# Performance work log

Hardware: AMD Instinct MI355X
Metric: run time of the kernel (lower is better)

The kernel has to match this reference:

```python
import jax, jax.numpy as jnp
import numpy as np

BN_EPS = 1e-5
LN_EPS = 1e-5


def conv1d(x, w, b):
    # x: (B, Cin, L), w: (Cout, Cin, K) 'same' padding
    pad = (w.shape[-1] - 1) // 2
    y = jax.lax.conv_general_dilated(x, w, (1,), [(pad, pad)],
                                     dimension_numbers=('NCH', 'OIH', 'NCH'))
    return y + b[None, :, None]


def bn_eval(x, g, b):
    # BatchNorm1d in eval mode with running_mean=0, running_var=1
    scale = g / np.float32(np.sqrt(1.0 + BN_EPS))
    return x * scale[None, :, None] + b[None, :, None]


def dss_kernel(lam_re, lam_im, log_dt, W_re, W_im, L):
    # lam_*: (N,), log_dt: (H,), W_*: (2, H, N) -> K: (2, H, L) real
    Lam = -jnp.exp(lam_re) + 1j * lam_im                  # (N,) stable poles
    dt = jnp.exp(log_dt)                                   # (H,)
    dtL = dt[:, None] * Lam[None, :]                       # (H, N)
    # ZOH-style input discretization folded into W
    Wc = (W_re + 1j * W_im) * ((jnp.exp(dtL) - 1.0) / Lam[None, :])[None]  # (2,H,N)
    pos = jnp.arange(L, dtype=jnp.float32)
    E = jnp.exp(dtL[:, :, None] * pos[None, None, :])      # (H, N, L) complex Vandermonde
    return jnp.einsum('chn,hnl->chl', Wc, E).real          # (2, H, L)


def dss_layer(x, lam_re, lam_im, log_dt, W_re, W_im, D, out_w, out_b):
    # x: (B, H, L) transposed DSS block, bidirectional, postact='glu'
    B, H, L = x.shape
    K = dss_kernel(lam_re, lam_im, log_dt, W_re, W_im, L)  # (2, H, L)
    zpad = jnp.zeros_like(K[0])
    k = (jnp.concatenate([K[0], zpad], -1) +
         jnp.concatenate([zpad, K[1][..., ::-1]], -1))     # (H, 2L) bidirectional kernel
    k_f = jnp.fft.rfft(k, axis=-1)                          # (H, L+1)
    u_f = jnp.fft.rfft(x, n=2 * L, axis=-1)                 # (B, H, L+1)
    y = jnp.fft.irfft(k_f[None] * u_f, n=2 * L, axis=-1)[..., :L]
    y = y + D[None, :, None] * x                            # skip term
    y = jax.nn.gelu(y, approximate=False)
    y = jnp.einsum('oh,bhl->bol', out_w, y) + out_b[None, :, None]  # (B, 2H, L)
    a, g = jnp.split(y, 2, axis=1)
    return a * jax.nn.sigmoid(g)                            # GLU -> (B, H, L)


def layernorm_ch(x, g, b):
    # LayerNorm over channel dim of (B, H, L)
    mu = x.mean(axis=1, keepdims=True)
    var = ((x - mu) ** 2).mean(axis=1, keepdims=True)
    return (x - mu) / jnp.sqrt(var + LN_EPS) * g[None, :, None] + b[None, :, None]


def reference(x, enc_w, enc_b, rn_w1, rn_b1, rn_g1, rn_be1, rn_w2, rn_b2, rn_g2,
              rn_be2, lam_re, lam_im, log_dt, W_re, W_im, D, out_w, out_b,
              ln_g, ln_b, dec_w, dec_b):
    x = conv1d(x, enc_w, enc_b)                             # (B, H, L)
    for i in range(rn_w1.shape[0]):                         # resnet L1Blocks
        z = jax.nn.relu(bn_eval(conv1d(x, rn_w1[i], rn_b1[i]), rn_g1[i], rn_be1[i]))
        z = bn_eval(conv1d(z, rn_w2[i], rn_b2[i]), rn_g2[i], rn_be2[i])
        x = jax.nn.relu(z + x)
    for i in range(lam_re.shape[0]):                        # DSS blocks (post-norm)
        z = dss_layer(x, lam_re[i], lam_im[i], log_dt[i], W_re[i], W_im[i],
                      D[i], out_w[i], out_b[i])
        x = layernorm_ch(z + x, ln_g[i], ln_b[i])
    return conv1d(x, dec_w, dec_b)                          # (B, d_output, L)


def setup_inputs() -> dict:
    key = jax.random.key(0)
    ks = jax.random.split(key, 12)
    B, L, H, N = 16, 8192, 128, 32
    nl, nr = 4, 3
    f = lambda k, shape, s=1.0: jax.random.normal(k, shape, dtype=jnp.float32) * np.float32(s)
    x = f(ks[0], (B, 5, L))
    enc_w = f(ks[1], (H, 5, 15), 1.0 / np.sqrt(5 * 15)); enc_b = jnp.zeros((H,), jnp.float32)
    rn_w1 = f(ks[2], (nr, H, H, 7), 1.0 / np.sqrt(H * 7)); rn_b1 = jnp.zeros((nr, H), jnp.float32)
    rn_w2 = f(ks[3], (nr, H, H, 7), 1.0 / np.sqrt(H * 7)); rn_b2 = jnp.zeros((nr, H), jnp.float32)
    rn_g1 = jnp.ones((nr, H), jnp.float32); rn_be1 = jnp.zeros((nr, H), jnp.float32)
    rn_g2 = jnp.ones((nr, H), jnp.float32); rn_be2 = jnp.zeros((nr, H), jnp.float32)
    lam_re = f(ks[4], (nl, N), 0.5)
    lam_im = jnp.pi * jnp.arange(N, dtype=jnp.float32)[None, :] * jnp.ones((nl, 1), jnp.float32)
    log_dt = f(ks[5], (nl, H), 0.5) - 4.0
    W_re = f(ks[6], (nl, 2, H, N), 1.0 / np.sqrt(N))
    W_im = f(ks[7], (nl, 2, H, N), 1.0 / np.sqrt(N))
    D = f(ks[8], (nl, H))
    out_w = f(ks[9], (nl, 2 * H, H), 1.0 / np.sqrt(H)); out_b = jnp.zeros((nl, 2 * H), jnp.float32)
    ln_g = jnp.ones((nl, H), jnp.float32); ln_b = jnp.zeros((nl, H), jnp.float32)
    dec_w = f(ks[10], (5, H, 15), 1.0 / np.sqrt(H * 15)); dec_b = jnp.zeros((5,), jnp.float32)
    return {'x': x, 'enc_w': enc_w, 'enc_b': enc_b, 'rn_w1': rn_w1, 'rn_b1': rn_b1,
            'rn_g1': rn_g1, 'rn_be1': rn_be1, 'rn_w2': rn_w2, 'rn_b2': rn_b2,
            'rn_g2': rn_g2, 'rn_be2': rn_be2, 'lam_re': lam_re, 'lam_im': lam_im,
            'log_dt': log_dt, 'W_re': W_re, 'W_im': W_im, 'D': D, 'out_w': out_w,
            'out_b': out_b, 'ln_g': ln_g, 'ln_b': ln_b, 'dec_w': dec_w, 'dec_b': dec_b}
```

## Files before the change

### kernel.cpp

```cpp
#include <hip/hip_runtime.h>
#include <hip/hip_bf16.h>


#define BN   16
#define HCH  128
#define LSEQ 8192
#define NST  32
#define NLAY 4
#define XT_BSTRIDE 2101248ull

typedef __attribute__((ext_vector_type(4))) float f32x4;
typedef __attribute__((ext_vector_type(8))) short short8;
typedef unsigned short u16;
typedef unsigned int   u32;

struct __align__(8) U2 { u32 x, y; };
struct __align__(16) US8 { u16 v[8]; };
struct __align__(8) US4 { u16 v[4]; };

__device__ __forceinline__ u16 f2bf(float f){
  union { float f; u32 u; } v; v.f = f;
  u32 u = v.u;
  return (u16)((u + 0x7fffu + ((u >> 16) & 1u)) >> 16);
}
__device__ __forceinline__ float bf2f(u32 lo16){
  union { u32 u; float f; } v; v.u = lo16 << 16; return v.f;
}
__device__ __forceinline__ float geluf(float v){
  return 0.5f * v * (1.0f + erff(v * 0.70710678118654752f));
}

#define GLDS16(g, l) \
  __builtin_amdgcn_global_load_lds((const __attribute__((address_space(1))) u32*)(g), \
                                   (__attribute__((address_space(3))) u32*)(l), 16, 0, 0)

__global__ void k_xpad(u16* xTs){
  int b = blockIdx.x, t = threadIdx.x;
  char* base = (char*)xTs + (size_t)b * XT_BSTRIDE;
  int r = t >> 4;
  int row = (r < 8) ? r : (8192 + r);
  f32x4 z = {0.f, 0.f, 0.f, 0.f};
  *(f32x4*)(base + (size_t)row * 256 + (size_t)(t & 15) * 16) = z;
}

__global__ void k_wxform(const float* __restrict__ w1, const float* __restrict__ w2, u16* __restrict__ wswz){
  int idx = blockIdx.x * 256 + threadIdx.x;
  if (idx >= 6 * 128 * 896) return;
  int conv = idx / (128 * 896);
  int rem  = idx % (128 * 896);
  int co = rem / 896, K = rem % 896;
  int k = K >> 7, ci = K & 127;
  const float* src = (conv & 1) ? w2 : w1;
  int blk = conv >> 1;
  float v = src[(((size_t)blk * 128 + co) * 128 + ci) * 7 + k];
  int chunk = K >> 6, j = K & 63;
  size_t byteoff = (size_t)conv * 229376 + (size_t)chunk * 16384 + (size_t)co * 128
                 + (u32)((j * 2) ^ ((co & 7) << 4));
  *(u16*)((char*)wswz + byteoff) = f2bf(v);
}

__global__ void k_wdec(const float* __restrict__ dw, u16* __restrict__ wd){
  int idx = blockIdx.x * 256 + threadIdx.x;
  if (idx >= 16 * 1920) return;
  int co = idx / 1920, K = idx % 1920;
  int k = K >> 7, ci = K & 127;
  float v = (co < 5) ? dw[((size_t)co * 128 + ci) * 15 + k] : 0.f;
  size_t byteoff = (size_t)co * 3840 + (u32)((K * 2) ^ ((co & 7) << 4));
  *(u16*)((char*)wd + byteoff) = f2bf(v);
}

__global__ void k_wglu(const float* __restrict__ ow, u16* __restrict__ wg){
  int idx = blockIdx.x * 256 + threadIdx.x;
  if (idx >= NLAY * 256 * 128) return;
  int layer = idx >> 15;
  int rem = idx & 32767;
  int q = rem >> 7, k = rem & 127;
  int row = (q & 1) ? (128 + (q >> 1)) : (q >> 1);
  float v = ow[((size_t)layer * 256 + row) * 128 + k];
  u16 hb = f2bf(v);
  u16 lb = f2bf(v - bf2f(hb));
  int a_hi = k >> 6, kk = k & 63;
  size_t base = (size_t)layer * 131072 + (size_t)q * 128 + (u32)((kk * 2) ^ ((q & 7) << 4));
  *(u16*)((char*)wg + base + (size_t)a_hi * 32768) = hb;
  *(u16*)((char*)wg + base + (size_t)(2 + a_hi) * 32768) = lb;
}

__global__ void k_dssprep(const float* __restrict__ lam_re, const float* __restrict__ lam_im,
                          const float* __restrict__ log_dt, const float* __restrict__ W_re,
                          const float* __restrict__ W_im, float* __restrict__ dssp){
  int idx = blockIdx.x * 256 + threadIdx.x;
  if (idx >= NLAY * HCH * NST) return;
  int layer = idx / (HCH * NST);
  int hn = idx % (HCH * NST);
  int h = hn / NST, n = hn % NST;
  float Lre = -expf(lam_re[layer * NST + n]);
  float Lim = lam_im[layer * NST + n];
  float dt  = expf(log_dt[layer * HCH + h]);
  float are = dt * Lre, aim = dt * Lim;
  float er = expf(are);
  float rre = er * cosf(aim);
  float rim = er * sinf(aim);
  float nre = rre - 1.f, nim = rim;
  float den = 1.f / (Lre * Lre + Lim * Lim);
  float fre = (nre * Lre + nim * Lim) * den;
  float fim = (nim * Lre - nre * Lim) * den;
  float* base = dssp + (size_t)layer * 6 * HCH * NST;
  base[(0 * HCH + h) * NST + n] = rre;
  base[(1 * HCH + h) * NST + n] = rim;
  #pragma unroll
  for (int cc = 0; cc < 2; ++cc){
    float wr_ = W_re[(((size_t)layer * 2 + cc) * HCH + h) * NST + n];
    float wi_ = W_im[(((size_t)layer * 2 + cc) * HCH + h) * NST + n];
    base[((2 + 2 * cc) * HCH + h) * NST + n] = wr_ * fre - wi_ * fim;
    base[((3 + 2 * cc) * HCH + h) * NST + n] = wr_ * fim + wi_ * fre;
  }
}

__global__ __launch_bounds__(256) void k_mats(const float* __restrict__ pp,
                                              u16* __restrict__ A1c, u16* __restrict__ A2c,
                                              float* __restrict__ rC){
  int h = blockIdx.x, t = threadIdx.x;
  __shared__ float pre[129][33], pim[129][33];
  __shared__ float w0re[32], w0im[32], w1re[32], w1im[32];
  __shared__ float tf[128], tb[128];
  if (t < 32){
    int n = t;
    float rre = pp[(0 * HCH + h) * NST + n], rim = pp[(1 * HCH + h) * NST + n];
    w0re[n] = pp[(2 * HCH + h) * NST + n]; w0im[n] = pp[(3 * HCH + h) * NST + n];
    w1re[n] = pp[(4 * HCH + h) * NST + n]; w1im[n] = pp[(5 * HCH + h) * NST + n];
    float pr = 1.f, pi = 0.f;
    pre[0][n] = 1.f; pim[0][n] = 0.f;
    for (int p = 1; p <= 128; ++p){
      float nr = pr * rre - pi * rim;
      float ni = pr * rim + pi * rre;
      pr = nr; pi = ni;
      pre[p][n] = pr; pim[p][n] = pi;
    }
    rC[h * 64 + 2 * n] = pr; rC[h * 64 + 2 * n + 1] = pi;
  }
  __syncthreads();
  if (t < 128){
    float s = 0.f;
    for (int n = 0; n < 32; ++n) s += w0re[n] * pre[t][n] - w0im[n] * pim[t][n];
    tf[t] = s;
  } else {
    int d = t - 128;
    if (d == 0) tb[0] = 0.f;
    else {
      float s = 0.f;
      for (int n = 0; n < 32; ++n) s += w1re[n] * pre[d - 1][n] - w1im[n] * pim[d - 1][n];
      tb[d] = s;
    }
  }
  __syncthreads();
  for (int idx = t; idx < 4 * 128 * 64; idx += 256){
    int a = idx >> 13, rem = idx & 8191, q = rem >> 6, k = rem & 63;
    int j = (a & 1) * 64 + k;
    int n, p; float wr_, wi_;
    if (q < 64){ n = q >> 1; p = 127 - j; wr_ = w0re[n]; wi_ = w0im[n]; }
    else       { n = (q - 64) >> 1; p = j; wr_ = w1re[n]; wi_ = w1im[n]; }
    float pr = pre[p][n], pi = pim[p][n];
    float v = (q & 1) ? (wr_ * pi + wi_ * pr) : (wr_ * pr - wi_ * pi);
    u16 hb = f2bf(v);
    u16 ob = (a < 2) ? hb : f2bf(v - bf2f(hb));
    *(u16*)((char*)A1c + (size_t)h * 65536 + (size_t)a * 16384 + (size_t)q * 128
            + (u32)((k * 2) ^ ((q & 7) << 4))) = ob;
  }
  for (int idx = t; idx < 8 * 128 * 64; idx += 256){
    int a = idx >> 13, rem = idx & 8191, i = rem >> 6, k = rem & 63;
    float v; bool lo;
    if (a < 4){
      int colT = (a & 1) * 64 + k;
      v = (i >= colT) ? tf[i - colT] : tb[colT - i];
      lo = (a >= 2);
    } else {
      int n = k >> 1;
      int p = (a < 6) ? (i + 1) : (127 - i);
      v = (k & 1) ? -pim[p][n] : pre[p][n];
      lo = (a == 5) || (a == 7);
    }
    u16 hb = f2bf(v);
    u16 ob = lo ? f2bf(v - bf2f(hb)) : hb;
    *(u16*)((char*)A2c + (size_t)h * 131072 + (size_t)a * 16384 + (size_t)i * 128
            + (u32)((k * 2) ^ ((i & 7) << 4))) = ob;
  }
}

__global__ __launch_bounds__(128) void k_enc(const float* __restrict__ xin, const float* __restrict__ w,
                                             const float* __restrict__ bias, float* __restrict__ X){
  int b = blockIdx.y, l0 = blockIdx.x * 64;
  int t = threadIdx.x;
  __shared__ float xs[5][78];
  for (int i = t; i < 5 * 78; i += 128){
    int ci = i / 78, j = i % 78;
    int l = l0 - 7 + j;
    xs[ci][j] = (l >= 0 && l < LSEQ) ? xin[((size_t)b * 5 + ci) * LSEQ + l] : 0.f;
  }
  float wreg[75];
  #pragma unroll
  for (int i = 0; i < 75; ++i) wreg[i] = w[t * 75 + i];
  float bc = bias[t];
  __syncthreads();
  size_t orow = ((size_t)b * HCH + t) * LSEQ + l0;
  for (int gb = 0; gb < 8; ++gb){
    float acc[8] = {0, 0, 0, 0, 0, 0, 0, 0};
    #pragma unroll
    for (int ci = 0; ci < 5; ++ci){
      #pragma unroll
      for (int k = 0; k < 15; ++k){
        float wv = wreg[ci * 15 + k];
        #pragma unroll
        for (int j = 0; j < 8; ++j)
          acc[j] = fmaf(wv, xs[ci][gb * 8 + j + k], acc[j]);
      }
    }
    f32x4 o0 = {acc[0] + bc, acc[1] + bc, acc[2] + bc, acc[3] + bc};
    f32x4 o1 = {acc[4] + bc, acc[5] + bc, acc[6] + bc, acc[7] + bc};
    *(f32x4*)&X[orow + gb * 8]     = o0;
    *(f32x4*)&X[orow + gb * 8 + 4] = o1;
  }
}

__global__ __launch_bounds__(256) void k_xform(const float* __restrict__ Xin, u16* __restrict__ xTs){
  int b = blockIdx.y, l0 = blockIdx.x * 64;
  int t = threadIdx.x;
  __shared__ float tile[128][65];
  #pragma unroll
  for (int it = 0; it < 32; ++it){
    int idx = t + it * 256;
    int ci = idx >> 6, j = idx & 63;
    tile[ci][j] = Xin[((size_t)b * HCH + ci) * LSEQ + l0 + j];
  }
  __syncthreads();
  int rl = t >> 2, q = t & 3;
  int l = l0 + rl;
  char* rowp = (char*)xTs + (size_t)b * XT_BSTRIDE + (size_t)(l + 8) * 256;
  u32 key = ((u32)l & 7u) << 4;
  #pragma unroll
  for (int ii = 0; ii < 8; ++ii){
    int c0 = q * 32 + ii * 4;
    U2 val;
    val.x = (u32)f2bf(tile[c0 + 0][rl]) | ((u32)f2bf(tile[c0 + 1][rl]) << 16);
    val.y = (u32)f2bf(tile[c0 + 2][rl]) | ((u32)f2bf(tile[c0 + 3][rl]) << 16);
    *(U2*)(rowp + (((u32)(c0 * 2)) ^ key)) = val;
  }
}

__global__ __launch_bounds__(256, 2) void k_conv(
    const u16* __restrict__ xTs, const u16* __restrict__ wcv,
    const float* __restrict__ bng, const float* __restrict__ bnb, const float* __restrict__ bnbe,
    const float* __restrict__ Xres, float* __restrict__ Xout, u16* __restrict__ xTsOut)
{
  int b = blockIdx.y, l0 = blockIdx.x * 128;
  int tid = threadIdx.x, lane = tid & 63, wv = tid >> 6;
  int wr = wv >> 1, wc = wv & 1;
  int lan15 = lane & 15, lhi = lane >> 4;

  __shared__ alignas(16) u16 xt[144 * 128];
  __shared__ alignas(16) u16 wch[2][128 * 64];

  const char* xsrc = (const char*)xTs + (size_t)b * XT_BSTRIDE + (size_t)l0 * 256;
  #pragma unroll
  for (int is = 0; is < 9; ++is){
    int off = is * 4096 + wv * 1024;
    GLDS16(xsrc + off + (lane << 4), (char*)xt + off);
  }
  {
    const char* wsrc = (const char*)wcv;
    #pragma unroll
    for (int is = 0; is < 4; ++is){
      int off = is * 4096 + wv * 1024;
      GLDS16(wsrc + off + (lane << 4), (char*)&wch[0][0] + off);
    }
  }
  asm volatile("s_waitcnt vmcnt(0)" ::: "memory");
  __syncthreads();

  f32x4 acc[4][4];
  #pragma unroll
  for (int i = 0; i < 4; ++i)
    #pragma unroll
    for (int j = 0; j < 4; ++j) acc[i][j] = (f32x4){0.f, 0.f, 0.f, 0.f};

  for (int c = 0; c < 14; ++c){
    int cur = c & 1;
    if (c < 13){
      const char* wsrc = (const char*)wcv + (size_t)(c + 1) * 16384;
      #pragma unroll
      for (int is = 0; is < 4; ++is){
        int off = is * 4096 + wv * 1024;
        GLDS16(wsrc + off + (lane << 4), (char*)&wch[cur ^ 1][0] + off);
      }
    }
    int k = c >> 1;
    const char* wb = (const char*)&wch[cur][0];
    #pragma unroll
    for (int ks = 0; ks < 2; ++ks){
      short8 af[4], bf[4];
      int j0 = ks * 32 + lhi * 8;
      #pragma unroll
      for (int mt = 0; mt < 4; ++mt){
        int co = wr * 64 + mt * 16 + lan15;
        af[mt] = *(const short8*)(wb + co * 128 + ((j0 * 2) ^ ((co & 7) << 4)));
      }
      int ci0 = (c & 1) * 64 + ks * 32 + lhi * 8;
      #pragma unroll
      for (int nt = 0; nt < 4; ++nt){
        int ll = wc * 64 + nt * 16 + lan15;
        int row = ll + k + 5;
        int lg = l0 + ll + k - 3;
        bf[nt] = *(const short8*)((const char*)xt + row * 256 + ((ci0 * 2) ^ ((lg & 7) << 4)));
      }
      #pragma unroll
      for (int mt = 0; mt < 4; ++mt)
        #pragma unroll
        for (int nt = 0; nt < 4; ++nt)
          acc[mt][nt] = __builtin_amdgcn_mfma_f32_16x16x32_bf16(af[mt], bf[nt], acc[mt][nt], 0, 0, 0);
    }
    asm volatile("s_waitcnt vmcnt(0)" ::: "memory");
    __syncthreads();
  }

  bool hasres = (Xres != nullptr);
  bool hasout = (Xout != nullptr);
  u16* tr = xt;
  #pragma unroll
  for (int mt = 0; mt < 4; ++mt){
    float A4[4], B4[4];
    int co0 = wr * 64 + mt * 16 + (lhi << 2);
    #pragma unroll
    for (int reg = 0; reg < 4; ++reg){
      A4[reg] = bng[co0 + reg] * 0.99999500003749968f;
      B4[reg] = fmaf(bnb[co0 + reg], A4[reg], bnbe[co0 + reg]);
    }
    #pragma unroll
    for (int nt = 0; nt < 4; ++nt){
      int ll = wc * 64 + nt * 16 + lan15;
      int l = l0 + ll;
      US4 o;
      #pragma unroll
      for (int reg = 0; reg < 4; ++reg){
        float v = fmaf(acc[mt][nt][reg], A4[reg], B4[reg]);
        if (hasres) v += Xres[((size_t)b * HCH + co0 + reg) * LSEQ + l];
        v = fmaxf(v, 0.f);
        if (hasout) Xout[((size_t)b * HCH + co0 + reg) * LSEQ + l] = v;
        o.v[reg] = f2bf(v);
      }
      *(US4*)((char*)tr + ll * 256 + (u32)((co0 * 2) ^ ((ll & 7) << 4))) = o;
    }
  }
  if (xTsOut){
    __syncthreads();
    int row = tid >> 1, half = tid & 1;
    const char* s = (const char*)tr + row * 256 + half * 128;
    char* d = (char*)xTsOut + (size_t)b * XT_BSTRIDE + (size_t)(l0 + row + 8) * 256 + half * 128;
    #pragma unroll
    for (int i = 0; i < 8; ++i)
      *(f32x4*)(d + i * 16) = *(const f32x4*)(s + i * 16);
  }
}

__device__ __forceinline__ void stage_x_tile(const float* __restrict__ X, int h, int ct,
                                             char* xh, char* xl, int t){
  int k8 = t & 15;
  int c0 = t >> 4;
  #pragma unroll
  for (int it = 0; it < 8; ++it){
    int col = c0 + it * 16;
    int c = ct * 8 + (col >> 4), b = col & 15;
    const float* src = X + ((size_t)b * HCH + h) * LSEQ + (size_t)c * 128 + k8 * 8;
    f32x4 v0 = *(const f32x4*)src;
    f32x4 v1 = *(const f32x4*)(src + 4);
    US8 hi, lo;
    #pragma unroll
    for (int e = 0; e < 4; ++e){
      u16 hb = f2bf(v0[e]);
      hi.v[e] = hb; lo.v[e] = f2bf(v0[e] - bf2f(hb));
      u16 hb2 = f2bf(v1[e]);
      hi.v[e + 4] = hb2; lo.v[e + 4] = f2bf(v1[e] - bf2f(hb2));
    }
    u32 off = (u32)col * 256 + (u32)((k8 * 16) ^ ((col & 7) << 4));
    *(US8*)(xh + off) = hi;
    *(US8*)(xl + off) = lo;
  }
}

__global__ __launch_bounds__(256) void k_dss1(const float* __restrict__ X,
                                              const u16* __restrict__ A1c,
                                              float* __restrict__ P){
  int h = blockIdx.x, ct = blockIdx.y;
  int tid = threadIdx.x, lane = tid & 63, wv = tid >> 6;
  int wr = wv >> 1, wc = wv & 1, lan15 = lane & 15, lhi = lane >> 4;
  __shared__ alignas(16) u16 bx[32768];
  __shared__ alignas(16) u16 ach[8192];

  stage_x_tile(X, h, ct, (char*)bx, (char*)bx + 32768, tid);
  const char* abase = (const char*)A1c + (size_t)h * 65536;

  f32x4 acc[4][4];
  #pragma unroll
  for (int i = 0; i < 4; ++i)
    #pragma unroll
    for (int j = 0; j < 4; ++j) acc[i][j] = (f32x4){0.f, 0.f, 0.f, 0.f};

  #pragma unroll
  for (int g = 0; g < 4; ++g){
    __syncthreads();
    const char* an = abase + (size_t)g * 16384;
    #pragma unroll
    for (int is = 0; is < 4; ++is){
      int off = is * 4096 + wv * 1024;
      GLDS16(an + off + (lane << 4), (char*)ach + off);
    }
    asm volatile("s_waitcnt vmcnt(0)" ::: "memory");
    __syncthreads();
    int kb0 = (g & 1) * 64;
    int npass = (g < 2) ? 2 : 1;
    for (int p = 0; p < npass; ++p){
      const char* bt = (const char*)bx + p * 32768;
      #pragma unroll
      for (int ks = 0; ks < 2; ++ks){
        int ka = ks * 32 + lhi * 8;
        short8 af[4], bf[4];
        #pragma unroll
        for (int mt = 0; mt < 4; ++mt){
          int q = wr * 64 + mt * 16 + lan15;
          af[mt] = *(const short8*)((const char*)ach + q * 128 + ((ka * 2) ^ ((q & 7) << 4)));
        }
        int kb = kb0 + ka;
        #pragma unroll
        for (int nt = 0; nt < 4; ++nt){
          int col = wc * 64 + nt * 16 + lan15;
          bf[nt] = *(const short8*)(bt + col * 256 + ((kb * 2) ^ ((col & 7) << 4)));
        }
        #pragma unroll
        for (int mt = 0; mt < 4; ++mt)
          #pragma unroll
          for (int nt = 0; nt < 4; ++nt)
            acc[mt][nt] = __builtin_amdgcn_mfma_f32_16x16x32_bf16(af[mt], bf[nt], acc[mt][nt], 0, 0, 0);
      }
    }
  }

  #pragma unroll
  for (int mt = 0; mt < 4; ++mt)
    #pragma unroll
    for (int nt = 0; nt < 4; ++nt){
      int col = ct * 128 + wc * 64 + nt * 16 + lan15;
      int q0 = wr * 64 + mt * 16 + (lhi << 2);
      *(f32x4*)&P[((size_t)h * 1024 + col) * 128 + q0] = acc[mt][nt];
    }
}

__global__ __launch_bounds__(256) void k_scan(const float* __restrict__ P,
                                              const float* __restrict__ rC,
                                              u16* __restrict__ Sf, u16* __restrict__ Sb){
  int part = blockIdx.x & 3, h = blockIdx.x >> 2;
  int t = threadIdx.x;
  int dir = part >> 1;
  int b = (part & 1) * 8 + (t >> 5);
  int n = t & 31;
  float rre = rC[h * 64 + 2 * n], rim = rC[h * 64 + 2 * n + 1];
  u16* SO = dir ? Sb : Sf;
  const float* pbase = P + (size_t)h * 131072 + (size_t)b * 128 + dir * 64 + 2 * n;
  float sre = 0.f, sim = 0.f;
  u32 key = ((u32)b & 7u) << 4;
  for (int ii = 0; ii < 64; ++ii){
    int c = dir ? (63 - ii) : ii;
    u16 hr = f2bf(sre), hm = f2bf(sim);
    u32 hw = (u32)hr | ((u32)hm << 16);
    u32 lw = (u32)f2bf(sre - bf2f(hr)) | ((u32)f2bf(sim - bf2f(hm)) << 16);
    char* sp = (char*)SO + ((size_t)(h * 8 + (c >> 3)) * 2) * 16384
             + (size_t)((c & 7) * 16 + b) * 128 + (u32)((4 * n) ^ key);
    *(u32*)sp = hw;
    *(u32*)(sp + 16384) = lw;
    const float* pp = pbase + (size_t)c * 2048;
    float pr = pp[0], pi = pp[1];
    float nr = rre * sre - rim * sim + pr;
    float ni = rre * sim + rim * sre + pi;
    sre = nr; sim = ni;
  }
}

__global__ __launch_bounds__(256) void k_dss2(const float* __restrict__ X,
                                              const u16* __restrict__ A2c,
                                              const u16* __restrict__ Sf,
                                              const u16* __restrict__ Sb,
                                              const float* __restrict__ Dv,
                                              float* __restrict__ G){
  int h = blockIdx.x, ct = blockIdx.y;
  int tid = threadIdx.x, lane = tid & 63, wv = tid >> 6;
  int wr = wv >> 1, wc = wv & 1, lan15 = lane & 15, lhi = lane >> 4;
  __shared__ alignas(16) u16 bx[32768];
  __shared__ alignas(16) u16 ach[8192];

  {
    const char* st0 = (const char*)Sf + ((size_t)(h * 8 + ct) * 2) * 16384;
    const char* st2 = (const char*)Sb + ((size_t)(h * 8 + ct) * 2) * 16384;
    const char* stile[4] = {st0, st0 + 16384, st2, st2 + 16384};
    #pragma unroll
    for (int tt = 0; tt < 4; ++tt){
      #pragma unroll
      for (int is = 0; is < 4; ++is){
        int off = is * 4096 + wv * 1024;
        GLDS16(stile[tt] + off + (lane << 4), (char*)bx + tt * 16384 + off);
      }
    }
  }
  const char* abase = (const char*)A2c + (size_t)h * 131072;

  f32x4 acc[4][4];
  #pragma unroll
  for (int i = 0; i < 4; ++i)
    #pragma unroll
    for (int j = 0; j < 4; ++j) acc[i][j] = (f32x4){0.f, 0.f, 0.f, 0.f};

  {
    const int bo0[4] = {0, 0, 32768, 32768};
    #pragma unroll
    for (int g = 0; g < 4; ++g){
      __syncthreads();
      const char* an = abase + (size_t)(4 + g) * 16384;
      #pragma unroll
      for (int is = 0; is < 4; ++is){
        int off = is * 4096 + wv * 1024;
        GLDS16(an + off + (lane << 4), (char*)ach + off);
      }
      asm volatile("s_waitcnt vmcnt(0)" ::: "memory");
      __syncthreads();
      int npass = (g & 1) ? 1 : 2;
      for (int p = 0; p < npass; ++p){
        const char* bt = (const char*)bx + bo0[g] + p * 16384;
        #pragma unroll
        for (int ks = 0; ks < 2; ++ks){
          int ka = ks * 32 + lhi * 8;
          short8 af[4], bf[4];
          #pragma unroll
          for (int mt = 0; mt < 4; ++mt){
            int i = wr * 64 + mt * 16 + lan15;
            af[mt] = *(const short8*)((const char*)ach + i * 128 + ((ka * 2) ^ ((i & 7) << 4)));
          }
          #pragma unroll
          for (int nt = 0; nt < 4; ++nt){
            int col = wc * 64 + nt * 16 + lan15;
            bf[nt] = *(const short8*)(bt + col * 128 + ((ka * 2) ^ ((col & 7) << 4)));
          }
          #pragma unroll
          for (int mt = 0; mt < 4; ++mt)
            #pragma unroll
            for (int nt = 0; nt < 4; ++nt)
              acc[mt][nt] = __builtin_amdgcn_mfma_f32_16x16x32_bf16(af[mt], bf[nt], acc[mt][nt], 0, 0, 0);
        }
      }
    }
  }
  __syncthreads();
  stage_x_tile(X, h, ct, (char*)bx, (char*)bx + 32768, tid);
  #pragma unroll
  for (int g = 0; g < 4; ++g){
    __syncthreads();
    const char* an = abase + (size_t)g * 16384;
    #pragma unroll
    for (int is = 0; is < 4; ++is){
      int off = is * 4096 + wv * 1024;
      GLDS16(an + off + (lane << 4), (char*)ach + off);
    }
    asm volatile("s_waitcnt vmcnt(0)" ::: "memory");
    __syncthreads();
    int kb0 = (g & 1) * 64;
    int npass = (g < 2) ? 2 : 1;
    for (int p = 0; p < npass; ++p){
      const char* bt = (const char*)bx + p * 32768;
      #pragma unroll
      for (int ks = 0; ks < 2; ++ks){
        int ka = ks * 32 + lhi * 8;
        short8 af[4], bf[4];
        #pragma unroll
        for (int mt = 0; mt < 4; ++mt){
          int i = wr * 64 + mt * 16 + lan15;
          af[mt] = *(const short8*)((const char*)ach + i * 128 + ((ka * 2) ^ ((i & 7) << 4)));
        }
        int kb = kb0 + ka;
        #pragma unroll
        for (int nt = 0; nt < 4; ++nt){
          int col = wc * 64 + nt * 16 + lan15;
          bf[nt] = *(const short8*)(bt + col * 256 + ((kb * 2) ^ ((col & 7) << 4)));
        }
        #pragma unroll
        for (int mt = 0; mt < 4; ++mt)
          #pragma unroll
          for (int nt = 0; nt < 4; ++nt)
            acc[mt][nt] = __builtin_amdgcn_mfma_f32_16x16x32_bf16(af[mt], bf[nt], acc[mt][nt], 0, 0, 0);
      }
    }
  }
  float Dh = Dv[h];
  #pragma unroll
  for (int mt = 0; mt < 4; ++mt)
    #pragma unroll
    for (int nt = 0; nt < 4; ++nt){
      int col = wc * 64 + nt * 16 + lan15;
      int c = ct * 8 + (col >> 4), b = col & 15;
      int i0 = wr * 64 + mt * 16 + (lhi << 2);
      u32 off = (u32)col * 256 + (u32)((2 * i0) ^ ((col & 7) << 4));
      US4 hx = *(const US4*)((const char*)bx + off);
      US4 lx = *(const US4*)((const char*)bx + 32768 + off);
      size_t base = ((size_t)b * HCH + h) * LSEQ + (size_t)c * 128 + i0;
      f32x4 ov;
      #pragma unroll
      for (int e = 0; e < 4; ++e){
        float xv = bf2f(hx.v[e]) + bf2f(lx.v[e]);
        ov[e] = geluf(acc[mt][nt][e] + Dh * xv);
      }
      *(f32x4*)&G[base] = ov;
    }
}

__global__ __launch_bounds__(256) void k_glu2(
    const float* __restrict__ G,
    const u16* __restrict__ Wg,
    const float* __restrict__ ob,
    const float* __restrict__ lng, const float* __restrict__ lnb,
    float* __restrict__ X)
{
  int b = blockIdx.y, l0 = blockIdx.x * 64;
  int tid = threadIdx.x, lane = tid & 63, wv = tid >> 6;
  int lan15 = lane & 15, lhi = lane >> 4;
  __shared__ alignas(16) u16 gt[2][64 * 128];
  __shared__ alignas(16) u16 ach[256 * 64];
  __shared__ float lnbuf[4][64][2];

  {
    int hp = tid & 63, lgrp = tid >> 6;
    const float* g0 = G + ((size_t)b * HCH + 2 * hp) * LSEQ + l0 + lgrp * 16;
    const float* g1 = g0 + LSEQ;
    #pragma unroll
    for (int j4 = 0; j4 < 4; ++j4){
      f32x4 r0 = *(const f32x4*)(g0 + j4 * 4);
      f32x4 r1 = *(const f32x4*)(g1 + j4 * 4);
      #pragma unroll
      for (int e = 0; e < 4; ++e){
        int l = lgrp * 16 + j4 * 4 + e;
        u16 h0 = f2bf(r0[e]), h1 = f2bf(r1[e]);
        u16 q0 = f2bf(r0[e] - bf2f(h0)), q1 = f2bf(r1[e] - bf2f(h1));
        u32 off = (u32)l * 256 + (((u32)hp * 4) ^ (((u32)l & 7u) << 4));
        *(u32*)((char*)&gt[0][0] + off) = (u32)h0 | ((u32)h1 << 16);
        *(u32*)((char*)&gt[1][0] + off) = (u32)q0 | ((u32)q1 << 16);
      }
    }
  }

  f32x4 acc[4][4];
  #pragma unroll
  for (int i = 0; i < 4; ++i)
    #pragma unroll
    for (int j = 0; j < 4; ++j) acc[i][j] = (f32x4){0.f, 0.f, 0.f, 0.f};

  const int asel[6] = {0, 1, 0, 1, 2, 3};
  const int bsel[6] = {0, 0, 1, 1, 0, 0};
  const int bk0 [6] = {0, 64, 0, 64, 0, 64};
  for (int s = 0; s < 6; ++s){
    __syncthreads();
    const char* an = (const char*)Wg + (size_t)asel[s] * 32768;
    #pragma unroll
    for (int is = 0; is < 8; ++is){
      int off = is * 4096 + wv * 1024;
      GLDS16(an + off + (lane << 4), (char*)ach + off);
    }
    asm volatile("s_waitcnt vmcnt(0)" ::: "memory");
    __syncthreads();
    const char* bt = (const char*)&gt[bsel[s]][0];
    #pragma unroll
    for (int ks = 0; ks < 2; ++ks){
      int ka = ks * 32 + lhi * 8;
      short8 af[4], bf[4];
      #pragma unroll
      for (int mt = 0; mt < 4; ++mt){
        int q = wv * 64 + mt * 16 + lan15;
        af[mt] = *(const short8*)((const char*)ach + q * 128 + ((ka * 2) ^ ((q & 7) << 4)));
      }
      int kb = bk0[s] + ka;
      #pragma unroll
      for (int nt = 0; nt < 4; ++nt){
        int col = nt * 16 + lan15;
        bf[nt] = *(const short8*)(bt + col * 256 + ((kb * 2) ^ ((col & 7) << 4)));
      }
      #pragma unroll
      for (int mt = 0; mt < 4; ++mt)
        #pragma unroll
        for (int nt = 0; nt < 4; ++nt)
          acc[mt][nt] = __builtin_amdgcn_mfma_f32_16x16x32_bf16(af[mt], bf[nt], acc[mt][nt], 0, 0, 0);
    }
  }

  float s1v[4] = {0, 0, 0, 0}, s2v[4] = {0, 0, 0, 0};
  float oba[4][2], obg[4][2];
  #pragma unroll
  for (int mt = 0; mt < 4; ++mt)
    #pragma unroll
    for (int e = 0; e < 2; ++e){
      int o = wv * 32 + mt * 8 + lhi * 2 + e;
      oba[mt][e] = ob[o]; obg[mt][e] = ob[o + 128];
    }
  #pragma unroll
  for (int nt = 0; nt < 4; ++nt){
    int l = l0 + nt * 16 + lan15;
    #pragma unroll
    for (int mt = 0; mt < 4; ++mt){
      #pragma unroll
      for (int e = 0; e < 2; ++e){
        int o = wv * 32 + mt * 8 + lhi * 2 + e;
        float a = acc[mt][nt][2 * e]     + oba[mt][e];
        float g = acc[mt][nt][2 * e + 1] + obg[mt][e];
        float z = a * (1.f / (1.f + expf(-g)));
        float u = z + X[((size_t)b * HCH + o) * LSEQ + l];
        acc[mt][nt][2 * e] = u;
        s1v[nt] += u; s2v[nt] += u * u;
      }
    }
  }
  #pragma unroll
  for (int nt = 0; nt < 4; ++nt){
    s1v[nt] += __shfl_xor(s1v[nt], 16, 64);
    s1v[nt] += __shfl_xor(s1v[nt], 32, 64);
    s2v[nt] += __shfl_xor(s2v[nt], 16, 64);
    s2v[nt] += __shfl_xor(s2v[nt], 32, 64);
  }
  if (lhi == 0){
    #pragma unroll
    for (int nt = 0; nt < 4; ++nt){
      lnbuf[wv][nt * 16 + lan15][0] = s1v[nt];
      lnbuf[wv][nt * 16 + lan15][1] = s2v[nt];
    }
  }
  __syncthreads();
  #pragma unroll
  for (int nt = 0; nt < 4; ++nt){
    int col = nt * 16 + lan15;
    float S1 = lnbuf[0][col][0] + lnbuf[1][col][0] + lnbuf[2][col][0] + lnbuf[3][col][0];
    float S2 = lnbuf[0][col][1] + lnbuf[1][col][1] + lnbuf[2][col][1] + lnbuf[3][col][1];
    float mu = S1 * (1.f / 128.f);
    float var = S2 * (1.f / 128.f) - mu * mu;
    float rs = rsqrtf(var + 1e-5f);
    int l = l0 + col;
    #pragma unroll
    for (int mt = 0; mt < 4; ++mt)
// ... 50 lines not shown
      int co = (lhi << 2) + reg;
      if (co < 5) out[((size_t)b * 5 + co) * LSEQ + l] = acc[nt][reg] + bias[co];
    }
  }
}

extern "C" void kernel_launch(void* const* d_in, const int* in_sizes, int n_in,
                              void* d_out, int out_size, void* d_ws, size_t ws_size,
                              hipStream_t stream){
  (void)in_sizes; (void)n_in; (void)out_size; (void)ws_size;
  const float* x_in   = (const float*)d_in[0];
  const float* enc_w  = (const float*)d_in[1];
  const float* enc_b  = (const float*)d_in[2];
  const float* rn_w1  = (const float*)d_in[3];
  const float* rn_b1  = (const float*)d_in[4];
  const float* rn_g1  = (const float*)d_in[5];
  const float* rn_be1 = (const float*)d_in[6];
  const float* rn_w2  = (const float*)d_in[7];
  const float* rn_b2  = (const float*)d_in[8];
  const float* rn_g2  = (const float*)d_in[9];
  const float* rn_be2 = (const float*)d_in[10];
  const float* lam_re = (const float*)d_in[11];
  const float* lam_im = (const float*)d_in[12];
  const float* log_dt = (const float*)d_in[13];
  const float* W_re   = (const float*)d_in[14];
  const float* W_im   = (const float*)d_in[15];
  const float* Dv     = (const float*)d_in[16];
  const float* out_w  = (const float*)d_in[17];
  const float* out_b  = (const float*)d_in[18];
  const float* ln_g   = (const float*)d_in[19];
  const float* ln_b   = (const float*)d_in[20];
  const float* dec_w  = (const float*)d_in[21];
  const float* dec_b  = (const float*)d_in[22];

  char* ws = (char*)d_ws;
  float* X    = (float*)(ws + 0ull);
  float* PG   = (float*)(ws + 67108864ull);
  u16*   xTsB = (u16*)  (ws + 67108864ull);
  u16*   Sf   = (u16*)  (ws + 134217728ull);
  u16*   Sb   = (u16*)  (ws + 167772160ull);
  u16*   xTsA = (u16*)  (ws + 134217728ull);
  u16*   A1c  = (u16*)  (ws + 201326592ull);
  u16*   A2c  = (u16*)  (ws + 209715200ull);
  u16*   wswz = (u16*)  (ws + 226492416ull);
  u16*   wdec = (u16*)  (ws + 227868672ull);
  float* dssp = (float*)(ws + 227930112ull);
  float* rC   = (float*)(ws + 228323328ull);
  u16*   wglu = (u16*)  (ws + 228356096ull);

  k_xpad<<<16, 256, 0, stream>>>(xTsA);
  k_xpad<<<16, 256, 0, stream>>>(xTsB);
  k_wxform<<<2688, 256, 0, stream>>>(rn_w1, rn_w2, wswz);
  k_wdec<<<120, 256, 0, stream>>>(dec_w, wdec);
  k_wglu<<<512, 256, 0, stream>>>(out_w, wglu);
  k_dssprep<<<64, 256, 0, stream>>>(lam_re, lam_im, log_dt, W_re, W_im, dssp);
  k_enc<<<dim3(128, 16), 128, 0, stream>>>(x_in, enc_w, enc_b, X);
  k_xform<<<dim3(128, 16), 256, 0, stream>>>(X, xTsA);

  for (int r = 0; r < 3; ++r){
    k_conv<<<dim3(64, 16), 256, 0, stream>>>(xTsA, (const u16*)((char*)wswz + (size_t)(2 * r) * 229376),
        rn_g1 + r * HCH, rn_b1 + r * HCH, rn_be1 + r * HCH, nullptr, nullptr, xTsB);
    k_conv<<<dim3(64, 16), 256, 0, stream>>>(xTsB, (const u16*)((char*)wswz + (size_t)(2 * r + 1) * 229376),
        rn_g2 + r * HCH, rn_b2 + r * HCH, rn_be2 + r * HCH, X, X, (r == 2) ? nullptr : xTsA);
  }
  for (int dl = 0; dl < NLAY; ++dl){
    k_mats<<<128, 256, 0, stream>>>(dssp + (size_t)dl * 6 * HCH * NST, A1c, A2c, rC);
    k_dss1<<<dim3(128, 8), 256, 0, stream>>>(X, A1c, PG);
    k_scan<<<512, 256, 0, stream>>>(PG, rC, Sf, Sb);
    k_dss2<<<dim3(128, 8), 256, 0, stream>>>(X, A2c, Sf, Sb, Dv + dl * HCH, PG);
    k_glu2<<<dim3(128, 16), 256, 0, stream>>>(PG, (const u16*)((char*)wglu + (size_t)dl * 131072),
        out_b + dl * 256, ln_g + dl * HCH, ln_b + dl * HCH, X);
  }
  k_xpad<<<16, 256, 0, stream>>>(xTsA);
  k_xform<<<dim3(128, 16), 256, 0, stream>>>(X, xTsA);
  k_dec2<<<dim3(64, 16), 256, 0, stream>>>(xTsA, wdec, dec_b, (float*)d_out);
}
```

Before: 1.472 ms.

## Pre-swizzle weight matrices into MFMA fragment order and load directly to registers

Weight/operator matrices for the conv, DSS and GLU GEMMs are now written in per-lane MFMA fragment order, so each wave loads its A fragments straight from global memory into registers with 16-byte loads. This removes the LDS staging buffers for A, the per-chunk barriers and the global_load_lds waits. Fragments are double-buffered in registers (afA/afB) so the next chunk's load overlaps the current MFMAs. The costs are higher register pressure (launch_bounds min-blocks hint dropped on k_conv) and redundant global reads of weights by waves sharing the same rows.

```diff
diff --git a/kernel.cpp b/kernel.cpp
--- a/kernel.cpp
+++ b/kernel.cpp
@@ -33,6 +33,26 @@
 #define GLDS16(g, l) \
   __builtin_amdgcn_global_load_lds((const __attribute__((address_space(1))) u32*)(g), \
                                    (__attribute__((address_space(3))) u32*)(l), 16, 0, 0)
+
+#define LOAD_FRAGS(F, BASE) do { \
+  _Pragma("unroll") for (int _ks = 0; _ks < 2; ++_ks) \
+    _Pragma("unroll") for (int _mt = 0; _mt < 4; ++_mt) \
+      F[_ks * 4 + _mt] = *(const short8*)((BASE) + _ks * 4096 + _mt * 1024); \
+} while (0)
+
+#define MFMA_PASS(F, BT, KB0, STRIDE) do { \
+  _Pragma("unroll") for (int _ks = 0; _ks < 2; ++_ks){ \
+    int _kb = (KB0) + _ks * 32 + lhi * 8; \
+    short8 _bf[4]; \
+    _Pragma("unroll") for (int _nt = 0; _nt < 4; ++_nt){ \
+      int _col = wc * 64 + _nt * 16 + lan15; \
+      _bf[_nt] = *(const short8*)((BT) + _col * (STRIDE) + (((_kb) * 2) ^ ((_col & 7) << 4))); \
+    } \
+    _Pragma("unroll") for (int _mt = 0; _mt < 4; ++_mt) \
+      _Pragma("unroll") for (int _nt = 0; _nt < 4; ++_nt) \
+        acc[_mt][_nt] = __builtin_amdgcn_mfma_f32_16x16x32_bf16(F[_ks * 4 + _mt], _bf[_nt], acc[_mt][_nt], 0, 0, 0); \
+  } \
+} while (0)
 
 __global__ void k_xpad(u16* xTs){
   int b = blockIdx.x, t = threadIdx.x;
@@ -43,20 +63,22 @@
   *(f32x4*)(base + (size_t)row * 256 + (size_t)(t & 15) * 16) = z;
 }
 
-__global__ void k_wxform(const float* __restrict__ w1, const float* __restrict__ w2, u16* __restrict__ wswz){
+__global__ void k_wxform(const float* __restrict__ w1, const float* __restrict__ w2, u16* __restrict__ wfr){
   int idx = blockIdx.x * 256 + threadIdx.x;
-  if (idx >= 6 * 128 * 896) return;
-  int conv = idx / (128 * 896);
-  int rem  = idx % (128 * 896);
-  int co = rem / 896, K = rem % 896;
+  if (idx >= 6 * 114688) return;
+  int e = idx & 7, r = idx >> 3;
+  int lane = r & 63; r >>= 6;
+  int mt = r & 3; r >>= 2;
+  int ks = r & 1; r >>= 1;
+  int wr = r & 1; r >>= 1;
+  int c = r % 14; int conv = r / 14;
+  int co = wr * 64 + mt * 16 + (lane & 15);
+  int K = c * 64 + ks * 32 + (lane >> 4) * 8 + e;
   int k = K >> 7, ci = K & 127;
   const float* src = (conv & 1) ? w2 : w1;
   int blk = conv >> 1;
   float v = src[(((size_t)blk * 128 + co) * 128 + ci) * 7 + k];
-  int chunk = K >> 6, j = K & 63;
-  size_t byteoff = (size_t)conv * 229376 + (size_t)chunk * 16384 + (size_t)co * 128
-                 + (u32)((j * 2) ^ ((co & 7) << 4));
-  *(u16*)((char*)wswz + byteoff) = f2bf(v);
+  wfr[idx] = f2bf(v);
 }
 
 __global__ void k_wdec(const float* __restrict__ dw, u16* __restrict__ wd){
@@ -71,18 +93,19 @@
 
 __global__ void k_wglu(const float* __restrict__ ow, u16* __restrict__ wg){
   int idx = blockIdx.x * 256 + threadIdx.x;
-  if (idx >= NLAY * 256 * 128) return;
-  int layer = idx >> 15;
-  int rem = idx & 32767;
-  int q = rem >> 7, k = rem & 127;
+  if (idx >= NLAY * 65536) return;
+  int e = idx & 7, r = idx >> 3;
+  int lane = r & 63; r >>= 6;
+  int mt = r & 3; r >>= 2;
+  int ks = r & 1; r >>= 1;
+  int wv = r & 3; r >>= 2;
+  int a = r & 3; int layer = r >> 2;
+  int q = wv * 64 + mt * 16 + (lane & 15);
+  int k = (a & 1) * 64 + ks * 32 + (lane >> 4) * 8 + e;
   int row = (q & 1) ? (128 + (q >> 1)) : (q >> 1);
   float v = ow[((size_t)layer * 256 + row) * 128 + k];
   u16 hb = f2bf(v);
-  u16 lb = f2bf(v - bf2f(hb));
-  int a_hi = k >> 6, kk = k & 63;
-  size_t base = (size_t)layer * 131072 + (size_t)q * 128 + (u32)((kk * 2) ^ ((q & 7) << 4));
-  *(u16*)((char*)wg + base + (size_t)a_hi * 32768) = hb;
-  *(u16*)((char*)wg + base + (size_t)(2 + a_hi) * 32768) = lb;
+  wg[idx] = (a < 2) ? hb : f2bf(v - bf2f(hb));
 }
 
 __global__ void k_dssprep(const float* __restrict__ lam_re, const float* __restrict__ lam_im,
@@ -153,36 +176,47 @@
     }
   }
   __syncthreads();
-  for (int idx = t; idx < 4 * 128 * 64; idx += 256){
-    int a = idx >> 13, rem = idx & 8191, q = rem >> 6, k = rem & 63;
-    int j = (a & 1) * 64 + k;
+  for (int idx = t; idx < 32768; idx += 256){
+    int e = idx & 7, r = idx >> 3;
+    int lane = r & 63; r >>= 6;
+    int mt = r & 3; r >>= 2;
+    int ks = r & 1; r >>= 1;
+    int wr = r & 1; r >>= 1;
+    int g = r;
+    int q = wr * 64 + mt * 16 + (lane & 15);
+    int j = (g & 1) * 64 + ks * 32 + (lane >> 4) * 8 + e;
     int n, p; float wr_, wi_;
     if (q < 64){ n = q >> 1; p = 127 - j; wr_ = w0re[n]; wi_ = w0im[n]; }
     else       { n = (q - 64) >> 1; p = j; wr_ = w1re[n]; wi_ = w1im[n]; }
     float pr = pre[p][n], pi = pim[p][n];
     float v = (q & 1) ? (wr_ * pi + wi_ * pr) : (wr_ * pr - wi_ * pi);
     u16 hb = f2bf(v);
-    u16 ob = (a < 2) ? hb : f2bf(v - bf2f(hb));
-    *(u16*)((char*)A1c + (size_t)h * 65536 + (size_t)a * 16384 + (size_t)q * 128
-            + (u32)((k * 2) ^ ((q & 7) << 4))) = ob;
-  }
-  for (int idx = t; idx < 8 * 128 * 64; idx += 256){
-    int a = idx >> 13, rem = idx & 8191, i = rem >> 6, k = rem & 63;
+    u16 ob = (g < 2) ? hb : f2bf(v - bf2f(hb));
+    *(u16*)((char*)A1c + (size_t)h * 65536 + (size_t)idx * 2) = ob;
+  }
+  for (int idx = t; idx < 65536; idx += 256){
+    int e = idx & 7, r = idx >> 3;
+    int lane = r & 63; r >>= 6;
+    int mt = r & 3; r >>= 2;
+    int ks = r & 1; r >>= 1;
+    int wr = r & 1; r >>= 1;
+    int a = r;
+    int i = wr * 64 + mt * 16 + (lane & 15);
+    int ka = ks * 32 + (lane >> 4) * 8 + e;
     float v; bool lo;
     if (a < 4){
-      int colT = (a & 1) * 64 + k;
-      v = (i >= colT) ? tf[i - colT] : tb[colT - i];
+      int j = (a & 1) * 64 + ka;
+      v = (i >= j) ? tf[i - j] : tb[j - i];
       lo = (a >= 2);
     } else {
-      int n = k >> 1;
+      int n = ka >> 1;
       int p = (a < 6) ? (i + 1) : (127 - i);
-      v = (k & 1) ? -pim[p][n] : pre[p][n];
+      v = (ka & 1) ? -pim[p][n] : pre[p][n];
       lo = (a == 5) || (a == 7);
     }
     u16 hb = f2bf(v);
     u16 ob = lo ? f2bf(v - bf2f(hb)) : hb;
-    *(u16*)((char*)A2c + (size_t)h * 131072 + (size_t)a * 16384 + (size_t)i * 128
-            + (u32)((k * 2) ^ ((i & 7) << 4))) = ob;
+    *(u16*)((char*)A2c + (size_t)h * 131072 + (size_t)idx * 2) = ob;
   }
 }
 
@@ -246,8 +280,8 @@
   }
 }
 
-__global__ __launch_bounds__(256, 2) void k_conv(
-    const u16* __restrict__ xTs, const u16* __restrict__ wcv,
+__global__ __launch_bounds__(256) void k_conv(
+    const u16* __restrict__ xTs, const u16* __restrict__ wfr,
     const float* __restrict__ bng, const float* __restrict__ bnb, const float* __restrict__ bnbe,
     const float* __restrict__ Xres, float* __restrict__ Xout, u16* __restrict__ xTsOut)
 {
@@ -257,7 +291,6 @@
   int lan15 = lane & 15, lhi = lane >> 4;
 
   __shared__ alignas(16) u16 xt[144 * 128];
-  __shared__ alignas(16) u16 wch[2][128 * 64];
 
   const char* xsrc = (const char*)xTs + (size_t)b * XT_BSTRIDE + (size_t)l0 * 256;
   #pragma unroll
@@ -265,14 +298,10 @@
     int off = is * 4096 + wv * 1024;
     GLDS16(xsrc + off + (lane << 4), (char*)xt + off);
   }
-  {
-    const char* wsrc = (const char*)wcv;
-    #pragma unroll
-    for (int is = 0; is < 4; ++is){
-      int off = is * 4096 + wv * 1024;
-      GLDS16(wsrc + off + (lane << 4), (char*)&wch[0][0] + off);
-    }
-  }
+  const char* wb = (const char*)wfr + (size_t)wr * 8192 + ((u32)lane << 4);
+  short8 afA[8], afB[8];
+  LOAD_FRAGS(afA, wb);
+  LOAD_FRAGS(afB, wb + 16384);
   asm volatile("s_waitcnt vmcnt(0)" ::: "memory");
   __syncthreads();
 
@@ -282,28 +311,12 @@
     #pragma unroll
     for (int j = 0; j < 4; ++j) acc[i][j] = (f32x4){0.f, 0.f, 0.f, 0.f};
 
-  for (int c = 0; c < 14; ++c){
-    int cur = c & 1;
-    if (c < 13){
-      const char* wsrc = (const char*)wcv + (size_t)(c + 1) * 16384;
-      #pragma unroll
-      for (int is = 0; is < 4; ++is){
-        int off = is * 4096 + wv * 1024;
-        GLDS16(wsrc + off + (lane << 4), (char*)&wch[cur ^ 1][0] + off);
-      }
-    }
+  for (int c = 0; c < 14; c += 2){
     int k = c >> 1;
-    const char* wb = (const char*)&wch[cur][0];
     #pragma unroll
     for (int ks = 0; ks < 2; ++ks){
-      short8 af[4], bf[4];
-      int j0 = ks * 32 + lhi * 8;
-      #pragma unroll
-      for (int mt = 0; mt < 4; ++mt){
-        int co = wr * 64 + mt * 16 + lan15;
-        af[mt] = *(const short8*)(wb + co * 128 + ((j0 * 2) ^ ((co & 7) << 4)));
-      }
-      int ci0 = (c & 1) * 64 + ks * 32 + lhi * 8;
+      int ci0 = ks * 32 + lhi * 8;
+      short8 bf[4];
       #pragma unroll
       for (int nt = 0; nt < 4; ++nt){
         int ll = wc * 64 + nt * 16 + lan15;
@@ -315,12 +328,30 @@
       for (int mt = 0; mt < 4; ++mt)
         #pragma unroll
         for (int nt = 0; nt < 4; ++nt)
-          acc[mt][nt] = __builtin_amdgcn_mfma_f32_16x16x32_bf16(af[mt], bf[nt], acc[mt][nt], 0, 0, 0);
-    }
-    asm volatile("s_waitcnt vmcnt(0)" ::: "memory");
-    __syncthreads();
-  }
-
+          acc[mt][nt] = __builtin_amdgcn_mfma_f32_16x16x32_bf16(afA[ks * 4 + mt], bf[nt], acc[mt][nt], 0, 0, 0);
+    }
+    if (c + 2 < 14) LOAD_FRAGS(afA, wb + (size_t)(c + 2) * 16384);
+    #pragma unroll
+    for (int ks = 0; ks < 2; ++ks){
+      int ci0 = 64 + ks * 32 + lhi * 8;
+      short8 bf[4];
+      #pragma unroll
+      for (int nt = 0; nt < 4; ++nt){
+        int ll = wc * 64 + nt * 16 + lan15;
+        int row = ll + k + 5;
+        int lg = l0 + ll + k - 3;
+        bf[nt] = *(const short8*)((const char*)xt + row * 256 + ((ci0 * 2) ^ ((lg & 7) << 4)));
+      }
+      #pragma unroll
+      for (int mt = 0; mt < 4; ++mt)
+        #pragma unroll
+        for (int nt = 0; nt < 4; ++nt)
+          acc[mt][nt] = __builtin_amdgcn_mfma_f32_16x16x32_bf16(afB[ks * 4 + mt], bf[nt], acc[mt][nt], 0, 0, 0);
+    }
+    if (c + 3 < 14) LOAD_FRAGS(afB, wb + (size_t)(c + 3) * 16384);
+  }
+
+  __syncthreads();
   bool hasres = (Xres != nullptr);
   bool hasout = (Xout != nullptr);
   u16* tr = xt;
@@ -392,10 +423,13 @@
   int tid = threadIdx.x, lane = tid & 63, wv = tid >> 6;
   int wr = wv >> 1, wc = wv & 1, lan15 = lane & 15, lhi = lane >> 4;
   __shared__ alignas(16) u16 bx[32768];
-  __shared__ alignas(16) u16 ach[8192];
 
   stage_x_tile(X, h, ct, (char*)bx, (char*)bx + 32768, tid);
-  const char* abase = (const char*)A1c + (size_t)h * 65536;
+  const char* wb = (const char*)A1c + (size_t)h * 65536 + (size_t)wr * 8192 + ((u32)lane << 4);
+  short8 fA[8], fB[8];
+  LOAD_FRAGS(fA, wb);
+  LOAD_FRAGS(fB, wb + 16384);
+  __syncthreads();
 
   f32x4 acc[4][4];
   #pragma unroll
@@ -403,44 +437,16 @@
     #pragma unroll
     for (int j = 0; j < 4; ++j) acc[i][j] = (f32x4){0.f, 0.f, 0.f, 0.f};
 
-  #pragma unroll
-  for (int g = 0; g < 4; ++g){
-    __syncthreads();
-    const char* an = abase + (size_t)g * 16384;
-    #pragma unroll
-    for (int is = 0; is < 4; ++is){
-      int off = is * 4096 + wv * 1024;
-      GLDS16(an + off + (lane << 4), (char*)ach + off);
-    }
-    asm volatile("s_waitcnt vmcnt(0)" ::: "memory");
-    __syncthreads();
-    int kb0 = (g & 1) * 64;
-    int npass = (g < 2) ? 2 : 1;
-    for (int p = 0; p < npass; ++p){
-      const char* bt = (const char*)bx + p * 32768;
-      #pragma unroll
-      for (int ks = 0; ks < 2; ++ks){
-        int ka = ks * 32 + lhi * 8;
-        short8 af[4], bf[4];
-        #pragma unroll
-        for (int mt = 0; mt < 4; ++mt){
-          int q = wr * 64 + mt * 16 + lan15;
-          af[mt] = *(const short8*)((const char*)ach + q * 128 + ((ka * 2) ^ ((q & 7) << 4)));
-        }
-        int kb = kb0 + ka;
-        #pragma unroll
-        for (int nt = 0; nt < 4; ++nt){
-          int col = wc * 64 + nt * 16 + lan15;
-          bf[nt] = *(const short8*)(bt + col * 256 + ((kb * 2) ^ ((col & 7) << 4)));
-        }
-        #pragma unroll
-        for (int mt = 0; mt < 4; ++mt)
-          #pragma unroll
-          for (int nt = 0; nt < 4; ++nt)
-            acc[mt][nt] = __builtin_amdgcn_mfma_f32_16x16x32_bf16(af[mt], bf[nt], acc[mt][nt], 0, 0, 0);
-      }
-    }
-  }
+  const char* xh = (const char*)bx;
+  const char* xl = (const char*)bx + 32768;
+  MFMA_PASS(fA, xh, 0, 256);
+  MFMA_PASS(fA, xl, 0, 256);
+  LOAD_FRAGS(fA, wb + 2 * 16384);
+  MFMA_PASS(fB, xh, 64, 256);
+  MFMA_PASS(fB, xl, 64, 256);
+  LOAD_FRAGS(fB, wb + 3 * 16384);
+  MFMA_PASS(fA, xh, 0, 256);
+  MFMA_PASS(fB, xh, 64, 256);
 
   #pragma unroll
   for (int mt = 0; mt < 4; ++mt)
@@ -492,7 +498,6 @@
   int tid = threadIdx.x, lane = tid & 63, wv = tid >> 6;
   int wr = wv >> 1, wc = wv & 1, lan15 = lane & 15, lhi = lane >> 4;
   __shared__ alignas(16) u16 bx[32768];
-  __shared__ alignas(16) u16 ach[8192];
 
   {
     const char* st0 = (const char*)Sf + ((size_t)(h * 8 + ct) * 2) * 16384;
@@ -507,7 +512,12 @@
       }
     }
   }
-  const char* abase = (const char*)A2c + (size_t)h * 131072;
+  const char* wb = (const char*)A2c + (size_t)h * 131072 + (size_t)wr * 8192 + ((u32)lane << 4);
+  short8 fA[8], fB[8];
+  LOAD_FRAGS(fA, wb + 4 * 16384);
+  LOAD_FRAGS(fB, wb + 5 * 16384);
+  asm volatile("s_waitcnt vmcnt(0)" ::: "memory");
+  __syncthreads();
 
   f32x4 acc[4][4];
   #pragma unroll
@@ -515,85 +525,36 @@
     #pragma unroll
     for (int j = 0; j < 4; ++j) acc[i][j] = (f32x4){0.f, 0.f, 0.f, 0.f};
 
-  {
-    const int bo0[4] = {0, 0, 32768, 32768};
-    #pragma unroll
-    for (int g = 0; g < 4; ++g){
-      __syncthreads();
-      const char* an = abase + (size_t)(4 + g) * 16384;
-      #pragma unroll
-      for (int is = 0; is < 4; ++is){
-        int off = is * 4096 + wv * 1024;
-        GLDS16(an + off + (lane << 4), (char*)ach + off);
-      }
-      asm volatile("s_waitcnt vmcnt(0)" ::: "memory");
-      __syncthreads();
-      int npass = (g & 1) ? 1 : 2;
-      for (int p = 0; p < npass; ++p){
-        const char* bt = (const char*)bx + bo0[g] + p * 16384;
-        #pragma unroll
-        for (int ks = 0; ks < 2; ++ks){
-          int ka = ks * 32 + lhi * 8;
-          short8 af[4], bf[4];
-          #pragma unroll
-          for (int mt = 0; mt < 4; ++mt){
-            int i = wr * 64 + mt * 16 + lan15;
-            af[mt] = *(const short8*)((const char*)ach + i * 128 + ((ka * 2) ^ ((i & 7) << 4)));
-          }
-          #pragma unroll
-          for (int nt = 0; nt < 4; ++nt){
-            int col = wc * 64 + nt * 16 + lan15;
-            bf[nt] = *(const short8*)(bt + col * 128 + ((ka * 2) ^ ((col & 7) << 4)));
-          }
-          #pragma unroll
-          for (int mt = 0; mt < 4; ++mt)
-            #pragma unroll
-            for (int nt = 0; nt < 4; ++nt)
-              acc[mt][nt] = __builtin_amdgcn_mfma_f32_16x16x32_bf16(af[mt], bf[nt], acc[mt][nt], 0, 0, 0);
-        }
-      }
-    }
-  }
+  const char* sfh = (const char*)bx;
+  const char* sfl = (const char*)bx + 16384;
+  const char* sbh = (const char*)bx + 32768;
+  const char* sbl = (const char*)bx + 49152;
+  MFMA_PASS(fA, sfh, 0, 128);
+  MFMA_PASS(fA, sfl, 0, 128);
+  LOAD_FRAGS(fA, wb + 6 * 16384);
+  MFMA_PASS(fB, sfh, 0, 128);
+  LOAD_FRAGS(fB, wb + 7 * 16384);
+  MFMA_PASS(fA, sbh, 0, 128);
+  MFMA_PASS(fA, sbl, 0, 128);
+  LOAD_FRAGS(fA, wb);
+  MFMA_PASS(fB, sbh, 0, 128);
+  LOAD_FRAGS(fB, wb + 16384);
+
   __syncthreads();
   stage_x_tile(X, h, ct, (char*)bx, (char*)bx + 32768, tid);
-  #pragma unroll
-  for (int g = 0; g < 4; ++g){
-    __syncthreads();
-    const char* an = abase + (size_t)g * 16384;
-    #pragma unroll
-    for (int is = 0; is < 4; ++is){
-      int off = is * 4096 + wv * 1024;
-      GLDS16(an + off + (lane << 4), (char*)ach + off);
-    }
-    asm volatile("s_waitcnt vmcnt(0)" ::: "memory");
-    __syncthreads();
-    int kb0 = (g & 1) * 64;
-    int npass = (g < 2) ? 2 : 1;
-    for (int p = 0; p < npass; ++p){
-      const char* bt = (const char*)bx + p * 32768;
-      #pragma unroll
-      for (int ks = 0; ks < 2; ++ks){
-        int ka = ks * 32 + lhi * 8;
-        short8 af[4], bf[4];
-        #pragma unroll
-        for (int mt = 0; mt < 4; ++mt){
-          int i = wr * 64 + mt * 16 + lan15;
-          af[mt] = *(const short8*)((const char*)ach + i * 128 + ((ka * 2) ^ ((i & 7) << 4)));
-        }
-        int kb = kb0 + ka;
-        #pragma unroll
-        for (int nt = 0; nt < 4; ++nt){
-          int col = wc * 64 + nt * 16 + lan15;
-          bf[nt] = *(const short8*)(bt + col * 256 + ((kb * 2) ^ ((col & 7) << 4)));
-        }
-        #pragma unroll
-        for (int mt = 0; mt < 4; ++mt)
-          #pragma unroll
-          for (int nt = 0; nt < 4; ++nt)
-            acc[mt][nt] = __builtin_amdgcn_mfma_f32_16x16x32_bf16(af[mt], bf[nt], acc[mt][nt], 0, 0, 0);
-      }
-    }
-  }
+  __syncthreads();
+
+  const char* xh = (const char*)bx;
+  const char* xl = (const char*)bx + 32768;
+  MFMA_PASS(fA, xh, 0, 256);
+  MFMA_PASS(fA, xl, 0, 256);
+  LOAD_FRAGS(fA, wb + 2 * 16384);
+  MFMA_PASS(fB, xh, 64, 256);
+  MFMA_PASS(fB, xl, 64, 256);
+  LOAD_FRAGS(fB, wb + 3 * 16384);
+  MFMA_PASS(fA, xh, 0, 256);
+  MFMA_PASS(fB, xh, 64, 256);
+
   float Dh = Dv[h];
   #pragma unroll
   for (int mt = 0; mt < 4; ++mt)
@@ -626,8 +587,8 @@
   int b = blockIdx.y, l0 = blockIdx.x * 64;
   int tid = threadIdx.x, lane = tid & 63, wv = tid >> 6;
   int lan15 = lane & 15, lhi = lane >> 4;
+  int wc = 0;
   __shared__ alignas(16) u16 gt[2][64 * 128];
-  __shared__ alignas(16) u16 ach[256 * 64];
   __shared__ float lnbuf[4][64][2];
 
   {
@@ -649,6 +610,11 @@
       }
     }
   }
+  const char* wb = (const char*)Wg + (size_t)wv * 8192 + ((u32)lane << 4);
+  short8 fA[8], fB[8];
+  LOAD_FRAGS(fA, wb);
+  LOAD_FRAGS(fB, wb + 32768);
+  __syncthreads();
 
   f32x4 acc[4][4];
   #pragma unroll
@@ -656,42 +622,16 @@
     #pragma unroll
     for (int j = 0; j < 4; ++j) acc[i][j] = (f32x4){0.f, 0.f, 0.f, 0.f};
 
-  const int asel[6] = {0, 1, 0, 1, 2, 3};
-  const int bsel[6] = {0, 0, 1, 1, 0, 0};
-  const int bk0 [6] = {0, 64, 0, 64, 0, 64};
-  for (int s = 0; s < 6; ++s){
-    __syncthreads();
-    const char* an = (const char*)Wg + (size_t)asel[s] * 32768;
-    #pragma unroll
-    for (int is = 0; is < 8; ++is){
-      int off = is * 4096 + wv * 1024;
-      GLDS16(an + off + (lane << 4), (char*)ach + off);
-    }
-    asm volatile("s_waitcnt vmcnt(0)" ::: "memory");
-    __syncthreads();
-    const char* bt = (const char*)&gt[bsel[s]][0];
-    #pragma unroll
-    for (int ks = 0; ks < 2; ++ks){
-      int ka = ks * 32 + lhi * 8;
-      short8 af[4], bf[4];
-      #pragma unroll
-      for (int mt = 0; mt < 4; ++mt){
-        int q = wv * 64 + mt * 16 + lan15;
-        af[mt] = *(const short8*)((const char*)ach + q * 128 + ((ka * 2) ^ ((q & 7) << 4)));
-      }
-      int kb = bk0[s] + ka;
-      #pragma unroll
-      for (int nt = 0; nt < 4; ++nt){
-        int col = nt * 16 + lan15;
-        bf[nt] = *(const short8*)(bt + col * 256 + ((kb * 2) ^ ((col & 7) << 4)));
-      }
-      #pragma unroll
-      for (int mt = 0; mt < 4; ++mt)
-        #pragma unroll
-        for (int nt = 0; nt < 4; ++nt)
-          acc[mt][nt] = __builtin_amdgcn_mfma_f32_16x16x32_bf16(af[mt], bf[nt], acc[mt][nt], 0, 0, 0);
-    }
-  }
+  const char* gh = (const char*)&gt[0][0];
+  const char* gl = (const char*)&gt[1][0];
+  MFMA_PASS(fA, gh, 0, 256);
+  MFMA_PASS(fA, gl, 0, 256);
+  LOAD_FRAGS(fA, wb + 2 * 32768);
+  MFMA_PASS(fB, gh, 64, 256);
+  MFMA_PASS(fB, gl, 64, 256);
+  LOAD_FRAGS(fB, wb + 3 * 32768);
+  MFMA_PASS(fA, gh, 0, 256);
+  MFMA_PASS(fB, gh, 64, 256);
 
   float s1v[4] = {0, 0, 0, 0}, s2v[4] = {0, 0, 0, 0};
   float oba[4][2], obg[4][2];
@@ -848,7 +788,7 @@
   k_xpad<<<16, 256, 0, stream>>>(xTsB);
   k_wxform<<<2688, 256, 0, stream>>>(rn_w1, rn_w2, wswz);
   k_wdec<<<120, 256, 0, stream>>>(dec_w, wdec);
-  k_wglu<<<512, 256, 0, stream>>>(out_w, wglu);
+  k_wglu<<<1024, 256, 0, stream>>>(out_w, wglu);
   k_dssprep<<<64, 256, 0, stream>>>(lam_re, lam_im, log_dt, W_re, W_im, dssp);
   k_enc<<<dim3(128, 16), 128, 0, stream>>>(x_in, enc_w, enc_b, X);
   k_xform<<<dim3(128, 16), 256, 0, stream>>>(X, xTsA);
```

Result: slower. 1.539 ms (+4.5%).
